# Kernel optimization log

Measured on AMD Instinct MI355X. Metric: run time of the kernel, lower is better.

The kernel has to match this reference:

```python
import jax, jax.numpy as jnp
import numpy as np

B, ID, OD = 4096, 2048, 1024


def _conv_softmax(x, w):
    # x: [..., L]; torch Conv1d(1,1,k=3,stride=1,pad=1,bias=False) then softmax(dim=-1)
    L = x.shape[-1]
    xp = jnp.pad(x, [(0, 0)] * (x.ndim - 1) + [(1, 1)])
    y = w[0] * xp[..., 0:L] + w[1] * xp[..., 1:L + 1] + w[2] * xp[..., 2:L + 2]
    return jax.nn.softmax(y, axis=-1)


def _lstm_cell(x, h, c, Wih, Whh, bih, bhh):
    # torch LSTMCell gate order: i, f, g, o
    g = x @ Wih.T + h @ Whh.T + (bih + bhh)
    i, f, gg, o = jnp.split(g, 4, axis=-1)
    c2 = jax.nn.sigmoid(f) * c + jax.nn.sigmoid(i) * jnp.tanh(gg)
    h2 = jax.nn.sigmoid(o) * jnp.tanh(c2)
    return h2, c2


def _lstm_params(key, in_dim, hid):
    k = 1.0 / np.sqrt(hid)
    ks = jax.random.split(key, 4)
    Wih = jax.random.uniform(ks[0], (4 * hid, in_dim), jnp.float32, -k, k)
    Whh = jax.random.uniform(ks[1], (4 * hid, hid), jnp.float32, -k, k)
    bih = jax.random.uniform(ks[2], (4 * hid,), jnp.float32, -k, k)
    bhh = jax.random.uniform(ks[3], (4 * hid,), jnp.float32, -k, k)
    return Wih, Whh, bih, bhh


def setup_inputs() -> dict:
    key = jax.random.key(0)
    ks = jax.random.split(key, 12)
    spec = jax.random.normal(ks[0], (B, ID), jnp.float32)
    Wih1, Whh1, bih1, bhh1 = _lstm_params(ks[1], ID, OD)
    Wih2, Whh2, bih2, bhh2 = _lstm_params(ks[2], ID // 2, OD // 2)
    Wih3, Whh3, bih3, bhh3 = _lstm_params(ks[3], ID // 4, OD // 4)
    Wih4, Whh4, bih4, bhh4 = _lstm_params(ks[4], ID // 8, OD // 8)
    ck = np.sqrt(1.0 / 3.0)  # Conv1d(1,1,3) init bound
    w2_1h = jax.random.uniform(ks[5], (3,), jnp.float32, -ck, ck)
    w2_1c = jax.random.uniform(ks[6], (3,), jnp.float32, -ck, ck)
    w3_2h = jax.random.uniform(ks[7], (3,), jnp.float32, -ck, ck)
    w3_2c = jax.random.uniform(ks[8], (3,), jnp.float32, -ck, ck)
    w4_3h = jax.random.uniform(ks[9], (3,), jnp.float32, -ck, ck)
    w4_3c = jax.random.uniform(ks[10], (3,), jnp.float32, -ck, ck)
    return dict(spec=spec,
                Wih1=Wih1, Whh1=Whh1, bih1=bih1, bhh1=bhh1,
                Wih2=Wih2, Whh2=Whh2, bih2=bih2, bhh2=bhh2,
                Wih3=Wih3, Whh3=Whh3, bih3=bih3, bhh3=bhh3,
                Wih4=Wih4, Whh4=Whh4, bih4=bih4, bhh4=bhh4,
                w2_1h=w2_1h, w2_1c=w2_1c, w3_2h=w3_2h, w3_2c=w3_2c,
                w4_3h=w4_3h, w4_3c=w4_3c)


def reference(spec, Wih1, Whh1, bih1, bhh1, Wih2, Whh2, bih2, bhh2,
              Wih3, Whh3, bih3, bhh3, Wih4, Whh4, bih4, bhh4,
              w2_1h, w2_1c, w3_2h, w3_2c, w4_3h, w4_3c):
    b = spec.shape[0]
    # Level 4: 8 independent steps, fresh zero state each (torch code passes no hidden)
    x4 = spec.reshape(b, 8, ID // 8)
    z4 = jnp.zeros((b, 8, OD // 8), spec.dtype)
    h4, c4 = _lstm_cell(x4, z4, z4, Wih4, Whh4, bih4, bhh4)   # [b,8,OD/8]
    hb4 = _conv_softmax(h4.reshape(b, 4, OD // 4), w4_3h)      # pairs -> [b,4,OD/4]
    cb4 = _conv_softmax(c4.reshape(b, 4, OD // 4), w4_3c)
    # Level 3: 4 independent steps seeded by level-4 blended states
    x3 = spec.reshape(b, 4, ID // 4)
    h3, c3 = _lstm_cell(x3, hb4, cb4, Wih3, Whh3, bih3, bhh3)  # [b,4,OD/4]
    hb3 = _conv_softmax(h3.reshape(b, 2, OD // 2), w3_2h)      # [b,2,OD/2]
    cb3 = _conv_softmax(c3.reshape(b, 2, OD // 2), w3_2c)
    # Level 2: 2 independent steps
    x2 = spec.reshape(b, 2, ID // 2)
    h2, c2 = _lstm_cell(x2, hb3, cb3, Wih2, Whh2, bih2, bhh2)  # [b,2,OD/2]
    hb2 = _conv_softmax(h2.reshape(b, OD), w2_1h)              # [b,OD]
    cb2 = _conv_softmax(c2.reshape(b, OD), w2_1c)
    # Level 1: single full-resolution step; forward returns out1 = h1
    h1, c1 = _lstm_cell(spec, hb2, cb2, Wih1, Whh1, bih1, bhh1)
    return h1
```

## Files before the change

kernel.cpp:

```cpp
#include <hip/hip_runtime.h>


typedef __bf16 bf16x8 __attribute__((ext_vector_type(8)));
typedef float f32x4 __attribute__((ext_vector_type(4)));
typedef unsigned short u16x4 __attribute__((ext_vector_type(4)));

#define AS1 __attribute__((address_space(1)))
#define AS3 __attribute__((address_space(3)))

__device__ __forceinline__ unsigned short f2bf(float f) {
    union { float f; unsigned int i; } v; v.f = f;
    unsigned int r = v.i + 0x7fffu + ((v.i >> 16) & 1u);
    return (unsigned short)(r >> 16);
}
__device__ __forceinline__ float sigm(float x) { return 1.f / (1.f + __expf(-x)); }
__device__ __forceinline__ float tanh_(float x) { float e = __expf(2.f * x); return 1.f - 2.f / (e + 1.f); }

__global__ __launch_bounds__(256) void cvt_spec3(
    const float* __restrict__ spec, unsigned short* __restrict__ sB,
    unsigned short* __restrict__ X, unsigned short* __restrict__ Y, long n4)
{
    const long stride = (long)gridDim.x * blockDim.x;
    for (long i = (long)blockIdx.x * blockDim.x + threadIdx.x; i < n4; i += stride) {
        const float4 v = ((const float4*)spec)[i];
        u16x4 o; o.x = f2bf(v.x); o.y = f2bf(v.y); o.z = f2bf(v.z); o.w = f2bf(v.w);
        ((u16x4*)sB)[i] = o;
        const long b = i >> 9;
        const int c4 = (int)(i & 511);
        *(u16x4*)(X + (b * 4 + (c4 >> 7)) * 768  + ((c4 & 127) << 2)) = o;
        *(u16x4*)(Y + (b * 2 + (c4 >> 8)) * 1536 + ((c4 & 255) << 2)) = o;
    }
}

__global__ __launch_bounds__(256) void cvt_specA(
    const float* __restrict__ spec, unsigned short* __restrict__ dst, long n4)
{
    const long stride = (long)gridDim.x * blockDim.x;
    for (long i = (long)blockIdx.x * blockDim.x + threadIdx.x; i < n4; i += stride) {
        const float4 v = ((const float4*)spec)[i];
        const long m = i >> 9;
        const int col = ((int)(i & 511)) << 2;
        u16x4 o; o.x = f2bf(v.x); o.y = f2bf(v.y); o.z = f2bf(v.z); o.w = f2bf(v.w);
        *(u16x4*)(dst + m * 3072 + col) = o;
    }
}

struct PSeg { const float* src; unsigned short* dst; long g0; int H; int kshift; int dstld; int dstcol; };
struct PArgs { PSeg s[7]; long total; };

__global__ __launch_bounds__(256) void cvt_permW_all(PArgs pa)
{
    const long stride = (long)gridDim.x * blockDim.x;
    for (long gi = (long)blockIdx.x * blockDim.x + threadIdx.x; gi < pa.total; gi += stride) {
        int si = 0;
#pragma unroll
        for (int k = 1; k < 7; ++k) si += (gi >= pa.s[k].g0);
        const PSeg sg = pa.s[si];
        const long i = gi - sg.g0;
        const int kq = 1 << sg.kshift;
        const int p = (int)(i >> sg.kshift);
        const int kk = ((int)i & (kq - 1)) << 2;
        const int o = ((p >> 6) << 4) | (p & 15);
        const int q = (p >> 4) & 3;
        const long r = (long)q * sg.H + o;
        const float4 v = *(const float4*)(sg.src + (r << (sg.kshift + 2)) + kk);
        u16x4 wv; wv.x = f2bf(v.x); wv.y = f2bf(v.y); wv.z = f2bf(v.z); wv.w = f2bf(v.w);
        *(u16x4*)(sg.dst + (long)p * sg.dstld + sg.dstcol + kk) = wv;
    }
}

__global__ __launch_bounds__(256) void bias_all(
    const float* __restrict__ bih1, const float* __restrict__ bhh1,
    const float* __restrict__ bih2, const float* __restrict__ bhh2,
    const float* __restrict__ bih3, const float* __restrict__ bhh3,
    const float* __restrict__ bih4, const float* __restrict__ bhh4,
    float* __restrict__ bs1, float* __restrict__ bs2,
    float* __restrict__ bs3, float* __restrict__ bs4)
{
    const int i = blockIdx.x * 256 + threadIdx.x;
    const float *bih, *bhh; float* dst; int H, j;
    if (i < 4096)      { bih = bih1; bhh = bhh1; dst = bs1; H = 1024; j = i; }
    else if (i < 6144) { bih = bih2; bhh = bhh2; dst = bs2; H = 512;  j = i - 4096; }
    else if (i < 7168) { bih = bih3; bhh = bhh3; dst = bs3; H = 256;  j = i - 6144; }
    else               { bih = bih4; bhh = bhh4; dst = bs4; H = 128;  j = i - 7168; }
    const int o = ((j >> 6) << 4) | (j & 15);
    const int q = (j >> 4) & 3;
    dst[j] = bih[q * H + o] + bhh[q * H + o];
}

#define QUAD(S, NS, BF)                                                                     \
    { _Pragma("unroll") for (int mi = 0; mi < 4; ++mi) {                                    \
        _Pragma("unroll") for (int ni = 0; ni < 2; ++ni) {                                  \
            acc[(S)*4+mi][(NS)*2+ni] = __builtin_amdgcn_mfma_f32_16x16x32_bf16(             \
                aF[mi][0], BF[ni][0], acc[(S)*4+mi][(NS)*2+ni], 0, 0, 0);                   \
            acc[(S)*4+mi][(NS)*2+ni] = __builtin_amdgcn_mfma_f32_16x16x32_bf16(             \
                aF[mi][1], BF[ni][1], acc[(S)*4+mi][(NS)*2+ni], 0, 0, 0);                   \
    } } }

#define GLL(gsrc, loff) __builtin_amdgcn_global_load_lds(                                   \
    (const AS1 void*)(gsrc), (AS3 void*)(lds + (loff)), 16, 0, 0)

#define FENCE asm volatile("" ::: "memory")

template<bool HAS_CIN, bool LAST>
__global__ __launch_bounds__(512, 2) void gemm8(
    const unsigned short* __restrict__ A, const unsigned short* __restrict__ W, const int K,
    const float* __restrict__ bsum, const float* __restrict__ Cin,
    float* __restrict__ Hout, float* __restrict__ Cout, const int H)
{
    __shared__ __align__(16) char lds[131072];
    const int t = threadIdx.x;
    const int w = t >> 6, l = t & 63;
    const int wr = w >> 2, wc = w & 3;

    const int GX = gridDim.x, GY = gridDim.y;
    const int nwg = GX * GY;
    const int bid = (int)blockIdx.y * GX + (int)blockIdx.x;
    const int swz = (bid & 7) * (nwg >> 3) + (bid >> 3);
    const int m0 = (swz / GY) * 256, n0 = (swz % GY) * 256;

    const int colsw = ((l & 7) ^ (l >> 3)) * 8;
    const size_t k128 = (size_t)128 * K;
    const size_t aoff0 = (size_t)(m0 + w * 16 + (l >> 3)) * K + colsw;
    const size_t aoff1 = aoff0 + (size_t)8 * K;
    const size_t boff0 = (size_t)(n0 + w * 16 + (l >> 3)) * K + colsw;
    const size_t boff1 = boff0 + (size_t)8 * K;
    const int sd0 = w * 2048 + l * 16;
    const int sd1 = sd0 + 1024;

    const int lr128 = (l & 15) * 128;
    const int sw0 = (((l >> 4)    ) ^ (l & 7)) * 16;
    const int sw1 = (((l >> 4) + 4) ^ (l & 7)) * 16;

    f32x4 acc[8][4];
#pragma unroll
    for (int i = 0; i < 8; ++i)
#pragma unroll
        for (int j = 0; j < 4; ++j) acc[i][j] = (f32x4){0.f, 0.f, 0.f, 0.f};

    const int NT = K >> 6;

    GLL(A + aoff0, sd0);                      GLL(A + aoff1, sd1);
    GLL(A + aoff0 + k128, 16384 + sd0);       GLL(A + aoff1 + k128, 16384 + sd1);
    GLL(W + boff0, 32768 + sd0);              GLL(W + boff1, 32768 + sd1);
    GLL(W + boff0 + k128, 49152 + sd0);       GLL(W + boff1 + k128, 49152 + sd1);
    GLL(W + boff0 + 64, 98304 + sd0);         GLL(W + boff1 + 64, 98304 + sd1);
    GLL(W + boff0 + k128 + 64, 114688 + sd0); GLL(W + boff1 + k128 + 64, 114688 + sd1);

    bf16x8 aF[4][2], bF0[2][2], bF1[2][2];

    for (int tt = 0; tt < NT; ++tt) {
        const int q = tt & 1, qn = q ^ 1;
        const int rbA = (q << 16) + (wr << 14) + lr128;
        const int rbB = (q << 16) + 32768 + wc * 8192 + lr128;
        const bool st1 = (tt + 1 < NT), st2 = (tt + 2 < NT);

        if (st1) { asm volatile("s_waitcnt vmcnt(4)" ::: "memory"); }
        else     { asm volatile("s_waitcnt vmcnt(0)" ::: "memory"); }
        __builtin_amdgcn_s_barrier();
        FENCE;

#pragma unroll
        for (int mi = 0; mi < 4; ++mi) {
            aF[mi][0] = *(const bf16x8*)(lds + rbA + mi * 2048 + sw0);
            aF[mi][1] = *(const bf16x8*)(lds + rbA + mi * 2048 + sw1);
        }
#pragma unroll
        for (int ni = 0; ni < 2; ++ni) {
            bF0[ni][0] = *(const bf16x8*)(lds + rbB + ni * 2048 + sw0);
            bF0[ni][1] = *(const bf16x8*)(lds + rbB + ni * 2048 + sw1);
            bF1[ni][0] = *(const bf16x8*)(lds + rbB + 4096 + ni * 2048 + sw0);
            bF1[ni][1] = *(const bf16x8*)(lds + rbB + 4096 + ni * 2048 + sw1);
        }
        if (st1) {
            const size_t ko1 = (size_t)(tt + 1) * 64;
            GLL(A + aoff0 + ko1, (qn << 16) + sd0);
            GLL(A + aoff1 + ko1, (qn << 16) + sd1);
            GLL(A + aoff0 + k128 + ko1, (qn << 16) + 16384 + sd0);
            GLL(A + aoff1 + k128 + ko1, (qn << 16) + 16384 + sd1);
        }
        __builtin_amdgcn_s_setprio(1);
        QUAD(0, 0, bF0);
        QUAD(0, 1, bF1);
        __builtin_amdgcn_s_setprio(0);
#pragma unroll
        for (int mi = 0; mi < 4; ++mi) {
            aF[mi][0] = *(const bf16x8*)(lds + rbA + 8192 + mi * 2048 + sw0);
            aF[mi][1] = *(const bf16x8*)(lds + rbA + 8192 + mi * 2048 + sw1);
        }
        __builtin_amdgcn_s_barrier();
        FENCE;

        if (st2) {
            const size_t ko2 = (size_t)(tt + 2) * 64;
            GLL(W + boff0 + ko2, (q << 16) + 32768 + sd0);
            GLL(W + boff1 + ko2, (q << 16) + 32768 + sd1);
            GLL(W + boff0 + k128 + ko2, (q << 16) + 49152 + sd0);
            GLL(W + boff1 + k128 + ko2, (q << 16) + 49152 + sd1);
        }
        __builtin_amdgcn_s_setprio(1);
        QUAD(1, 1, bF1);
        QUAD(1, 0, bF0);
        __builtin_amdgcn_s_setprio(0);
    }

    const int ocol = (n0 >> 6) * 16 + wc * 16 + (l & 15);
    const int bb = n0 + wc * 64 + (l & 15);
    const float b0 = bsum[bb], b1 = bsum[bb + 16], b2 = bsum[bb + 32], b3 = bsum[bb + 48];
    const int mrow0 = m0 + wr * 128 + (l >> 4) * 4;
#pragma unroll
    for (int mi = 0; mi < 8; ++mi)
#pragma unroll
        for (int j = 0; j < 4; ++j) {
            const size_t m = (size_t)(mrow0 + mi * 16 + j);
            const float gi = acc[mi][0][j] + b0;
            const float gf = acc[mi][1][j] + b1;
            const float gg = acc[mi][2][j] + b2;
            const float go = acc[mi][3][j] + b3;
            float c2 = sigm(gi) * tanh_(gg);
            if (HAS_CIN) c2 += sigm(gf) * Cin[m * H + ocol];
            const float h2 = sigm(go) * tanh_(c2);
            Hout[m * H + ocol] = h2;
            if (!LAST) Cout[m * H + ocol] = c2;
        }
}

template<int L>
__global__ __launch_bounds__(256) void conv_dual(
    const float* __restrict__ Hin, const float* __restrict__ Cin,
    const float* __restrict__ w3h, const float* __restrict__ w3c,
    unsigned short* __restrict__ Yb, int ldYb, float* __restrict__ cbuf)
{
    __shared__ float xs[L + 2];
    __shared__ float red[8];
    const int nrows = gridDim.x >> 1;
    const bool isC = (int)blockIdx.x >= nrows;
    const int row = isC ? ((int)blockIdx.x - nrows) : (int)blockIdx.x;
    const float* Xs = isC ? Cin : Hin;
    const float* w3 = isC ? w3c : w3h;
    const int t = threadIdx.x;
    const size_t base = (size_t)row * L;
    const float w0 = w3[0], w1 = w3[1], w2 = w3[2];
    if (t == 0) { xs[0] = 0.f; xs[L + 1] = 0.f; }
    for (int i = t; i < L; i += 256) xs[i + 1] = Xs[base + i];
    __syncthreads();
    constexpr int E = L / 256;
    float y[E];
    float vmax = -3.4e38f;
#pragma unroll
    for (int i = 0; i < E; ++i) {
        const int c = t + i * 256;
        y[i] = w0 * xs[c] + w1 * xs[c + 1] + w2 * xs[c + 2];
        vmax = fmaxf(vmax, y[i]);
    }
#pragma unroll
    for (int off = 32; off >= 1; off >>= 1) vmax = fmaxf(vmax, __shfl_xor(vmax, off));
    if ((t & 63) == 0) red[t >> 6] = vmax;
    __syncthreads();
    vmax = fmaxf(fmaxf(red[0], red[1]), fmaxf(red[2], red[3]));
    float s = 0.f;
#pragma unroll
    for (int i = 0; i < E; ++i) { y[i] = __expf(y[i] - vmax); s += y[i]; }
#pragma unroll
    for (int off = 32; off >= 1; off >>= 1) s += __shfl_xor(s, off);
    if ((t & 63) == 0) red[4 + (t >> 6)] = s;
    __syncthreads();
    const float inv = 1.f / (red[4] + red[5] + red[6] + red[7]);
#pragma unroll
    for (int i = 0; i < E; ++i) {
        const int c = t + i * 256;
        const float v = y[i] * inv;
        if (isC) cbuf[base + c] = v;
        else     Yb[(size_t)row * ldYb + c] = f2bf(v);
    }
}

extern "C" void kernel_launch(void* const* d_in, const int* in_sizes, int n_in,
                              void* d_out, int out_size, void* d_ws, size_t ws_size,
                              hipStream_t stream)
{
    (void)in_sizes; (void)n_in; (void)out_size; (void)ws_size;
    const float* spec  = (const float*)d_in[0];
    const float* Wih1  = (const float*)d_in[1];
    const float* Whh1  = (const float*)d_in[2];
    const float* bih1  = (const float*)d_in[3];
    const float* bhh1  = (const float*)d_in[4];
    const float* Wih2  = (const float*)d_in[5];
    const float* Whh2  = (const float*)d_in[6];
    const float* bih2  = (const float*)d_in[7];
    const float* bhh2  = (const float*)d_in[8];
    const float* Wih3  = (const float*)d_in[9];
    const float* Whh3  = (const float*)d_in[10];
    const float* bih3  = (const float*)d_in[11];
    const float* bhh3  = (const float*)d_in[12];
    const float* Wih4  = (const float*)d_in[13];
    const float* bih4  = (const float*)d_in[15];
    const float* bhh4  = (const float*)d_in[16];
    const float* w2_1h = (const float*)d_in[17];
    const float* w2_1c = (const float*)d_in[18];
    const float* w3_2h = (const float*)d_in[19];
    const float* w3_2c = (const float*)d_in[20];
    const float* w4_3h = (const float*)d_in[21];
    const float* w4_3c = (const float*)d_in[22];

    char* ws = (char*)d_ws;
    float*          h   = (float*)(ws + 0);
    float*          c   = (float*)(ws + (size_t)16777216);
    float*          cb  = (float*)(ws + (size_t)33554432);
    unsigned short* sB  = (unsigned short*)(ws + (size_t)50331648);
    unsigned short* X   = (unsigned short*)(ws + (size_t)67108864);
    unsigned short* Y   = (unsigned short*)(ws + (size_t)92274688);
    unsigned short* Wc1 = (unsigned short*)(ws + (size_t)117440512);
    unsigned short* Wc2 = (unsigned short*)(ws + (size_t)142606336);
    unsigned short* Wc3 = (unsigned short*)(ws + (size_t)148897792);
    unsigned short* W4  = (unsigned short*)(ws + (size_t)150470656);
    float*          bs1 = (float*)(ws + (size_t)150732800);
    float*          bs2 = bs1 + 4096;
    float*          bs3 = bs2 + 4096;
    float*          bs4 = bs3 + 4096;

    cvt_spec3<<<2048, 256, 0, stream>>>(spec, sB, X, Y, 2097152);
    PArgs pa;
    pa.s[0] = { Wih1, Wc1,       0, 1024, 9, 3072,    0 };
    pa.s[1] = { Whh1, Wc1, 2097152, 1024, 8, 3072, 2048 };
    pa.s[2] = { Wih2, Wc2, 3145728,  512, 8, 1536,    0 };
    pa.s[3] = { Whh2, Wc2, 3670016,  512, 7, 1536, 1024 };
    pa.s[4] = { Wih3, Wc3, 3932160,  256, 7,  768,    0 };
    pa.s[5] = { Whh3, Wc3, 4063232,  256, 6,  768,  512 };
    pa.s[6] = { Wih4, W4,  4128768,  128, 6,  256,    0 };
    pa.total = 4161536;
    cvt_permW_all<<<2048, 256, 0, stream>>>(pa);
    bias_all<<<30, 256, 0, stream>>>(bih1, bhh1, bih2, bhh2, bih3, bhh3, bih4, bhh4,
                                     bs1, bs2, bs3, bs4);

    gemm8<false, false><<<dim3(128, 2), 512, 0, stream>>>(sB, W4, 256, bs4, nullptr, h, c, 128);
    conv_dual<256><<<32768, 256, 0, stream>>>(h, c, w4_3h, w4_3c, X + 512, 768, cb);

    gemm8<true, false><<<dim3(64, 4), 512, 0, stream>>>(X, Wc3, 768, bs3, cb, h, c, 256);
    cvt_specA<<<2048, 256, 0, stream>>>(spec, X, 2097152);
    conv_dual<512><<<16384, 256, 0, stream>>>(h, c, w3_2h, w3_2c, Y + 1024, 1536, cb);

    gemm8<true, false><<<dim3(32, 8), 512, 0, stream>>>(Y, Wc2, 1536, bs2, cb, h, c, 512);
    conv_dual<1024><<<8192, 256, 0, stream>>>(h, c, w2_1h, w2_1c, X + 2048, 3072, cb);

    gemm8<true, true><<<dim3(16, 16), 512, 0, stream>>>(X, Wc1, 3072, bs1, cb, (float*)d_out, nullptr, 1024);
}
```

Measured before the change: 334.1 us.

## Switch LSTM GEMM to 32x32x16 MFMA with 4x2 wave layout and 32-wide gate interleave

```diff
diff --git a/kernel.cpp b/kernel.cpp
--- a/kernel.cpp
+++ b/kernel.cpp
@@ -2,7 +2,7 @@
 
 
 typedef __bf16 bf16x8 __attribute__((ext_vector_type(8)));
-typedef float f32x4 __attribute__((ext_vector_type(4)));
+typedef float f32x16 __attribute__((ext_vector_type(16)));
 typedef unsigned short u16x4 __attribute__((ext_vector_type(4)));
 
 #define AS1 __attribute__((address_space(1)))
@@ -60,8 +60,8 @@
         const int kq = 1 << sg.kshift;
         const int p = (int)(i >> sg.kshift);
         const int kk = ((int)i & (kq - 1)) << 2;
-        const int o = ((p >> 6) << 4) | (p & 15);
-        const int q = (p >> 4) & 3;
+        const int o = ((p >> 7) << 5) | (p & 31);
+        const int q = (p >> 5) & 3;
         const long r = (long)q * sg.H + o;
         const float4 v = *(const float4*)(sg.src + (r << (sg.kshift + 2)) + kk);
         u16x4 wv; wv.x = f2bf(v.x); wv.y = f2bf(v.y); wv.z = f2bf(v.z); wv.w = f2bf(v.w);
@@ -83,19 +83,10 @@
     else if (i < 6144) { bih = bih2; bhh = bhh2; dst = bs2; H = 512;  j = i - 4096; }
     else if (i < 7168) { bih = bih3; bhh = bhh3; dst = bs3; H = 256;  j = i - 6144; }
     else               { bih = bih4; bhh = bhh4; dst = bs4; H = 128;  j = i - 7168; }
-    const int o = ((j >> 6) << 4) | (j & 15);
-    const int q = (j >> 4) & 3;
+    const int o = ((j >> 7) << 5) | (j & 31);
+    const int q = (j >> 5) & 3;
     dst[j] = bih[q * H + o] + bhh[q * H + o];
 }
-
-#define QUAD(S, NS, BF)                                                                     \
-    { _Pragma("unroll") for (int mi = 0; mi < 4; ++mi) {                                    \
-        _Pragma("unroll") for (int ni = 0; ni < 2; ++ni) {                                  \
-            acc[(S)*4+mi][(NS)*2+ni] = __builtin_amdgcn_mfma_f32_16x16x32_bf16(             \
-                aF[mi][0], BF[ni][0], acc[(S)*4+mi][(NS)*2+ni], 0, 0, 0);                   \
-            acc[(S)*4+mi][(NS)*2+ni] = __builtin_amdgcn_mfma_f32_16x16x32_bf16(             \
-                aF[mi][1], BF[ni][1], acc[(S)*4+mi][(NS)*2+ni], 0, 0, 0);                   \
-    } } }
 
 #define GLL(gsrc, loff) __builtin_amdgcn_global_load_lds(                                   \
     (const AS1 void*)(gsrc), (AS3 void*)(lds + (loff)), 16, 0, 0)
@@ -111,7 +102,7 @@
     __shared__ __align__(16) char lds[131072];
     const int t = threadIdx.x;
     const int w = t >> 6, l = t & 63;
-    const int wr = w >> 2, wc = w & 3;
+    const int wr = w >> 1, wc = w & 1;
 
     const int GX = gridDim.x, GY = gridDim.y;
     const int nwg = GX * GY;
@@ -128,15 +119,20 @@
     const int sd0 = w * 2048 + l * 16;
     const int sd1 = sd0 + 1024;
 
-    const int lr128 = (l & 15) * 128;
-    const int sw0 = (((l >> 4)    ) ^ (l & 7)) * 16;
-    const int sw1 = (((l >> 4) + 4) ^ (l & 7)) * 16;
-
-    f32x4 acc[8][4];
-#pragma unroll
-    for (int i = 0; i < 8; ++i)
-#pragma unroll
-        for (int j = 0; j < 4; ++j) acc[i][j] = (f32x4){0.f, 0.f, 0.f, 0.f};
+    const int lrow = (l & 31) * 128;
+    int gsw[8];
+#pragma unroll
+    for (int ks = 0; ks < 4; ++ks) {
+        gsw[ks * 2]     = (((ks << 1) | (l >> 5)) ^ (l & 7)) << 4;
+    }
+
+    f32x16 acc[2][4];
+#pragma unroll
+    for (int i = 0; i < 2; ++i)
+#pragma unroll
+        for (int j = 0; j < 4; ++j)
+#pragma unroll
+            for (int e = 0; e < 16; ++e) acc[i][j][e] = 0.f;
 
     const int NT = K >> 6;
 
@@ -147,12 +143,12 @@
     GLL(W + boff0 + 64, 98304 + sd0);         GLL(W + boff1 + 64, 98304 + sd1);
     GLL(W + boff0 + k128 + 64, 114688 + sd0); GLL(W + boff1 + k128 + 64, 114688 + sd1);
 
-    bf16x8 aF[4][2], bF0[2][2], bF1[2][2];
+    bf16x8 aF[2][4], bF0[2][4], bF1[2][4];
 
     for (int tt = 0; tt < NT; ++tt) {
         const int q = tt & 1, qn = q ^ 1;
-        const int rbA = (q << 16) + (wr << 14) + lr128;
-        const int rbB = (q << 16) + 32768 + wc * 8192 + lr128;
+        const int rbA = (q << 16) + (wr << 13) + lrow;
+        const int rbB = (q << 16) + 32768 + (wc << 14) + lrow;
         const bool st1 = (tt + 1 < NT), st2 = (tt + 2 < NT);
 
         if (st1) { asm volatile("s_waitcnt vmcnt(4)" ::: "memory"); }
@@ -161,16 +157,13 @@
         FENCE;
 
 #pragma unroll
-        for (int mi = 0; mi < 4; ++mi) {
-            aF[mi][0] = *(const bf16x8*)(lds + rbA + mi * 2048 + sw0);
-            aF[mi][1] = *(const bf16x8*)(lds + rbA + mi * 2048 + sw1);
-        }
-#pragma unroll
-        for (int ni = 0; ni < 2; ++ni) {
-            bF0[ni][0] = *(const bf16x8*)(lds + rbB + ni * 2048 + sw0);
-            bF0[ni][1] = *(const bf16x8*)(lds + rbB + ni * 2048 + sw1);
-            bF1[ni][0] = *(const bf16x8*)(lds + rbB + 4096 + ni * 2048 + sw0);
-            bF1[ni][1] = *(const bf16x8*)(lds + rbB + 4096 + ni * 2048 + sw1);
+        for (int ks = 0; ks < 4; ++ks) {
+#pragma unroll
+            for (int mi = 0; mi < 2; ++mi)
+                aF[mi][ks] = *(const bf16x8*)(lds + rbA + (mi << 12) + gsw[ks * 2]);
+#pragma unroll
+            for (int ni = 0; ni < 2; ++ni)
+                bF0[ni][ks] = *(const bf16x8*)(lds + rbB + (ni << 12) + gsw[ks * 2]);
         }
         if (st1) {
             const size_t ko1 = (size_t)(tt + 1) * 64;
@@ -180,17 +173,23 @@
             GLL(A + aoff1 + k128 + ko1, (qn << 16) + 16384 + sd1);
         }
         __builtin_amdgcn_s_setprio(1);
-        QUAD(0, 0, bF0);
-        QUAD(0, 1, bF1);
+#pragma unroll
+        for (int ks = 0; ks < 4; ++ks)
+#pragma unroll
+            for (int mi = 0; mi < 2; ++mi)
+#pragma unroll
+                for (int ni = 0; ni < 2; ++ni)
+                    acc[mi][ni] = __builtin_amdgcn_mfma_f32_32x32x16_bf16(
+                        aF[mi][ks], bF0[ni][ks], acc[mi][ni], 0, 0, 0);
         __builtin_amdgcn_s_setprio(0);
-#pragma unroll
-        for (int mi = 0; mi < 4; ++mi) {
-            aF[mi][0] = *(const bf16x8*)(lds + rbA + 8192 + mi * 2048 + sw0);
-            aF[mi][1] = *(const bf16x8*)(lds + rbA + 8192 + mi * 2048 + sw1);
-        }
         __builtin_amdgcn_s_barrier();
         FENCE;
 
+#pragma unroll
+        for (int ks = 0; ks < 4; ++ks)
+#pragma unroll
+            for (int ni = 0; ni < 2; ++ni)
+                bF1[ni][ks] = *(const bf16x8*)(lds + rbB + ((ni + 2) << 12) + gsw[ks * 2]);
         if (st2) {
             const size_t ko2 = (size_t)(tt + 2) * 64;
             GLL(W + boff0 + ko2, (q << 16) + 32768 + sd0);
@@ -199,24 +198,33 @@
             GLL(W + boff1 + k128 + ko2, (q << 16) + 49152 + sd1);
         }
         __builtin_amdgcn_s_setprio(1);
-        QUAD(1, 1, bF1);
-        QUAD(1, 0, bF0);
+#pragma unroll
+        for (int ks = 0; ks < 4; ++ks)
+#pragma unroll
+            for (int mi = 0; mi < 2; ++mi)
+#pragma unroll
+                for (int ni = 0; ni < 2; ++ni)
+                    acc[mi][ni + 2] = __builtin_amdgcn_mfma_f32_32x32x16_bf16(
+                        aF[mi][ks], bF1[ni][ks], acc[mi][ni + 2], 0, 0, 0);
         __builtin_amdgcn_s_setprio(0);
     }
 
-    const int ocol = (n0 >> 6) * 16 + wc * 16 + (l & 15);
-    const int bb = n0 + wc * 64 + (l & 15);
-    const float b0 = bsum[bb], b1 = bsum[bb + 16], b2 = bsum[bb + 32], b3 = bsum[bb + 48];
-    const int mrow0 = m0 + wr * 128 + (l >> 4) * 4;
-#pragma unroll
-    for (int mi = 0; mi < 8; ++mi)
-#pragma unroll
-        for (int j = 0; j < 4; ++j) {
-            const size_t m = (size_t)(mrow0 + mi * 16 + j);
-            const float gi = acc[mi][0][j] + b0;
-            const float gf = acc[mi][1][j] + b1;
-            const float gg = acc[mi][2][j] + b2;
-            const float go = acc[mi][3][j] + b3;
+    const int ncol0 = n0 + (wc << 7);
+    const int ocol = ((ncol0 >> 7) << 5) + (l & 31);
+    const float b0 = bsum[ncol0 +      (l & 31)];
+    const float b1 = bsum[ncol0 + 32 + (l & 31)];
+    const float b2 = bsum[ncol0 + 64 + (l & 31)];
+    const float b3 = bsum[ncol0 + 96 + (l & 31)];
+    const int mrow0 = m0 + (wr << 6) + ((l >> 5) << 2);
+#pragma unroll
+    for (int mi = 0; mi < 2; ++mi)
+#pragma unroll
+        for (int reg = 0; reg < 16; ++reg) {
+            const size_t m = (size_t)(mrow0 + (mi << 5) + (reg & 3) + ((reg >> 2) << 3));
+            const float gi = acc[mi][0][reg] + b0;
+            const float gf = acc[mi][1][reg] + b1;
+            const float gg = acc[mi][2][reg] + b2;
+            const float go = acc[mi][3][reg] + b3;
             float c2 = sigm(gi) * tanh_(gg);
             if (HAS_CIN) c2 += sigm(gf) * Cin[m * H + ocol];
             const float h2 = sigm(go) * tanh_(c2);
```

After: 331.6 us. No clear change (-0.7%).
